# Kernel optimization log

Measured on AMD Instinct MI355X. Metric: run time of the kernel, lower is better.

The kernel has to match this reference:

```python
import jax, jax.numpy as jnp
import numpy as np

C = 512
REDUCTION = 8
POOLED_LEN = 256


def setup_inputs() -> dict:
    key = jax.random.key(0)
    k_x, k_w1, k_b1, k_w2, k_b2 = jax.random.split(key, 5)
    B, H, W = 32, 64, 64
    hid = C // REDUCTION  # 64
    fan1 = C + POOLED_LEN  # 768
    x = jax.random.normal(k_x, (B, C, H, W), dtype=jnp.float32)
    # torch nn.Linear default init: U(-1/sqrt(fan_in), 1/sqrt(fan_in))
    lim1 = 1.0 / np.sqrt(fan1)
    lim2 = 1.0 / np.sqrt(hid)
    fc1_w = jax.random.uniform(k_w1, (hid, fan1), jnp.float32, -lim1, lim1)
    fc1_b = jax.random.uniform(k_b1, (hid,), jnp.float32, -lim1, lim1)
    fc2_w = jax.random.uniform(k_w2, (1, hid), jnp.float32, -lim2, lim2)
    fc2_b = jax.random.uniform(k_b2, (1,), jnp.float32, -lim2, lim2)
    return {"x": x, "fc1_w": fc1_w, "fc1_b": fc1_b, "fc2_w": fc2_w, "fc2_b": fc2_b}


def reference(x, fc1_w, fc1_b, fc2_w, fc2_b):
    B, Ch, H, W = x.shape
    # spatial mean pool -> channel descriptor [B, C]
    x_c = x.mean(axis=(2, 3))
    # outer-product channel affinity [B, C, C]
    affinity = x_c[:, :, None] * x_c[:, None, :]
    # concat affinity with its transpose along last dim -> [B, C, 2C]
    r_i = jnp.concatenate([affinity, jnp.swapaxes(affinity, 1, 2)], axis=2)
    # adaptive_avg_pool1d(2C -> pooled_len): 2C divisible by pooled_len,
    # so it's exact uniform window averaging
    win = (2 * Ch) // POOLED_LEN
    r_i_pooled = r_i.reshape(B, Ch, POOLED_LEN, win).mean(axis=-1)
    # x_c broadcast along dim 1 -> [B, C, C]
    x_pooled = jnp.broadcast_to(x_c[:, None, :], (B, Ch, Ch))
    att_input = jnp.concatenate([x_pooled, r_i_pooled], axis=2)  # [B, C, C+pooled_len]
    s = jax.nn.relu(jnp.einsum('bcf,hf->bch', att_input, fc1_w) + fc1_b)
    a = jax.nn.sigmoid(jnp.einsum('bch,oh->bco', s, fc2_w) + fc2_b)  # [B, C, 1]
    return x * a[:, :, :, None]  # [B, C, 1, 1] broadcast
```

## Files before the change

kernel.cpp:

```cpp
#include <hip/hip_runtime.h>
#include <math.h>


#define B_  32
#define C_  512
#define HW_ 4096
#define ROWS_ (B_ * C_)

__global__ __launch_bounds__(256) void k_rowmean(const float* __restrict__ x,
                                                 float* __restrict__ xc) {
    const int row = blockIdx.x;
    const float4* xr = (const float4*)(x + (size_t)row * HW_);
    const int tid = threadIdx.x;
    float s = 0.f;
#pragma unroll
    for (int k = 0; k < 4; ++k) {
        float4 v = xr[tid + k * 256];
        s += (v.x + v.y) + (v.z + v.w);
    }
#pragma unroll
    for (int off = 32; off > 0; off >>= 1) s += __shfl_down(s, off, 64);
    __shared__ float wsum[4];
    const int lane = tid & 63, wave = tid >> 6;
    if (lane == 0) wsum[wave] = s;
    __syncthreads();
    if (tid == 0) {
        float t = (wsum[0] + wsum[1]) + (wsum[2] + wsum[3]);
        xc[row] = t * (1.0f / (float)HW_);
    }
}

__global__ __launch_bounds__(256) void k_att(const float* __restrict__ xc,
                                             const float* __restrict__ fc1w,
                                             const float* __restrict__ fc1b,
                                             const float* __restrict__ fc2w,
                                             const float* __restrict__ fc2b,
                                             float* __restrict__ a) {
    const int b = blockIdx.x;
    const int tid = threadIdx.x;
    __shared__ float xcs[C_];
    __shared__ float qs[128];
    __shared__ float p1[256], p2[256];
    __shared__ float s1[64], s2[64], w2s[64];

    xcs[tid]       = xc[b * C_ + tid];
    xcs[tid + 256] = xc[b * C_ + 256 + tid];
    if (tid < 64) w2s[tid] = fc2w[tid];
    __syncthreads();

    if (tid < 128) {
        qs[tid] = (xcs[4 * tid] + xcs[4 * tid + 1] + xcs[4 * tid + 2] + xcs[4 * tid + 3]) * 0.25f;
    }
    __syncthreads();

    const int h = tid & 63, part = tid >> 6;
    const float* w = fc1w + h * 768;
    float t1 = 0.f, t2 = 0.f;
    {
        const int f0 = part * 128;
#pragma unroll 8
        for (int f = 0; f < 128; ++f) t1 += xcs[f0 + f] * w[f0 + f];
        const int m0 = part * 32;
#pragma unroll 8
        for (int m = 0; m < 32; ++m) t2 += qs[m0 + m] * (w[512 + m0 + m] + w[640 + m0 + m]);
    }
    p1[tid] = t1;
    p2[tid] = t2;
    __syncthreads();
    if (tid < 64) {
        s1[tid] = (p1[tid] + p1[tid + 64]) + (p1[tid + 128] + p1[tid + 192]) + fc1b[tid];
        s2[tid] = (p2[tid] + p2[tid + 64]) + (p2[tid + 128] + p2[tid + 192]);
    }
    __syncthreads();

    const float bias2 = fc2b[0];
    for (int c = tid; c < C_; c += 256) {
        const float xv = xcs[c];
        float acc = bias2;
#pragma unroll 8
        for (int hh = 0; hh < 64; ++hh) {
            float z = s1[hh] + xv * s2[hh];
            acc += w2s[hh] * (z > 0.f ? z : 0.f);
        }
        a[b * C_ + c] = 1.0f / (1.0f + __expf(-acc));
    }
}

__global__ __launch_bounds__(256) void k_scale(const float* __restrict__ x,
                                               const float* __restrict__ a,
                                               float* __restrict__ out) {
    const int row = blockIdx.x;
    const float s = a[row];
    const float4* xr = (const float4*)(x + (size_t)row * HW_);
    float4* outr = (float4*)(out + (size_t)row * HW_);
    const int tid = threadIdx.x;
#pragma unroll
    for (int k = 0; k < 4; ++k) {
        float4 v = xr[tid + k * 256];
        v.x *= s; v.y *= s; v.z *= s; v.w *= s;
        outr[tid + k * 256] = v;
    }
}

extern "C" void kernel_launch(void* const* d_in, const int* in_sizes, int n_in,
                              void* d_out, int out_size, void* d_ws, size_t ws_size,
                              hipStream_t stream) {
    const float* x     = (const float*)d_in[0];
    const float* fc1_w = (const float*)d_in[1];
    const float* fc1_b = (const float*)d_in[2];
    const float* fc2_w = (const float*)d_in[3];
    const float* fc2_b = (const float*)d_in[4];
    float* out = (float*)d_out;

    float* xc = (float*)d_ws;
    float* a  = xc + ROWS_;

    k_rowmean<<<ROWS_, 256, 0, stream>>>(x, xc);
    k_att<<<B_, 256, 0, stream>>>(xc, fc1_w, fc1_b, fc2_w, fc2_b, a);
    k_scale<<<ROWS_, 256, 0, stream>>>(x, a, out);
}
```

Before: 491.9 us.

## Fuse attention MLP into scale kernel and use wave-per-row reductions

```diff
diff --git a/kernel.cpp b/kernel.cpp
--- a/kernel.cpp
+++ b/kernel.cpp
@@ -7,41 +7,43 @@
 #define HW_ 4096
 #define ROWS_ (B_ * C_)
 
+typedef float f32x4 __attribute__((ext_vector_type(4)));
+
 __global__ __launch_bounds__(256) void k_rowmean(const float* __restrict__ x,
                                                  float* __restrict__ xc) {
-    const int row = blockIdx.x;
-    const float4* xr = (const float4*)(x + (size_t)row * HW_);
-    const int tid = threadIdx.x;
+    const int lane = threadIdx.x & 63;
+    const int wave = threadIdx.x >> 6;
+    const int row  = blockIdx.x * 4 + wave;
+    const f32x4* xr = (const f32x4*)(x + (size_t)row * HW_);
     float s = 0.f;
 #pragma unroll
-    for (int k = 0; k < 4; ++k) {
-        float4 v = xr[tid + k * 256];
-        s += (v.x + v.y) + (v.z + v.w);
+    for (int j = 0; j < 16; ++j) {
+        f32x4 v = xr[lane + j * 64];
+        s += (v[0] + v[1]) + (v[2] + v[3]);
     }
 #pragma unroll
     for (int off = 32; off > 0; off >>= 1) s += __shfl_down(s, off, 64);
-    __shared__ float wsum[4];
-    const int lane = tid & 63, wave = tid >> 6;
-    if (lane == 0) wsum[wave] = s;
-    __syncthreads();
-    if (tid == 0) {
-        float t = (wsum[0] + wsum[1]) + (wsum[2] + wsum[3]);
-        xc[row] = t * (1.0f / (float)HW_);
-    }
+    if (lane == 0) xc[row] = s * (1.0f / (float)HW_);
 }
 
-__global__ __launch_bounds__(256) void k_att(const float* __restrict__ xc,
-                                             const float* __restrict__ fc1w,
-                                             const float* __restrict__ fc1b,
-                                             const float* __restrict__ fc2w,
-                                             const float* __restrict__ fc2b,
-                                             float* __restrict__ a) {
-    const int b = blockIdx.x;
+__global__ __launch_bounds__(256) void k_att_scale(
+        const float* __restrict__ x,
+        const float* __restrict__ xc,
+        const float* __restrict__ fc1w,
+        const float* __restrict__ fc1b,
+        const float* __restrict__ fc2w,
+        const float* __restrict__ fc2b,
+        float* __restrict__ out) {
     const int tid = threadIdx.x;
+    const int row_lo = ROWS_ - (int)(blockIdx.x + 1) * 16;
+    const int b  = row_lo / C_;
+    const int c0 = row_lo % C_;
+
     __shared__ float xcs[C_];
     __shared__ float qs[128];
     __shared__ float p1[256], p2[256];
     __shared__ float s1[64], s2[64], w2s[64];
+    __shared__ float as[16];
 
     xcs[tid]       = xc[b * C_ + tid];
     xcs[tid + 256] = xc[b * C_ + 256 + tid];
@@ -49,23 +51,25 @@
     __syncthreads();
 
     if (tid < 128) {
-        qs[tid] = (xcs[4 * tid] + xcs[4 * tid + 1] + xcs[4 * tid + 2] + xcs[4 * tid + 3]) * 0.25f;
+        qs[tid] = (xcs[4 * tid] + xcs[4 * tid + 1] +
+                   xcs[4 * tid + 2] + xcs[4 * tid + 3]) * 0.25f;
     }
     __syncthreads();
 
-    const int h = tid & 63, part = tid >> 6;
-    const float* w = fc1w + h * 768;
-    float t1 = 0.f, t2 = 0.f;
     {
+        const int h = tid & 63, part = tid >> 6;
+        const float* w = fc1w + h * 768;
+        float t1 = 0.f, t2 = 0.f;
         const int f0 = part * 128;
 #pragma unroll 8
         for (int f = 0; f < 128; ++f) t1 += xcs[f0 + f] * w[f0 + f];
         const int m0 = part * 32;
 #pragma unroll 8
-        for (int m = 0; m < 32; ++m) t2 += qs[m0 + m] * (w[512 + m0 + m] + w[640 + m0 + m]);
+        for (int m = 0; m < 32; ++m)
+            t2 += qs[m0 + m] * (w[512 + m0 + m] + w[640 + m0 + m]);
+        p1[tid] = t1;
+        p2[tid] = t2;
     }
-    p1[tid] = t1;
-    p2[tid] = t2;
     __syncthreads();
     if (tid < 64) {
         s1[tid] = (p1[tid] + p1[tid + 64]) + (p1[tid + 128] + p1[tid + 192]) + fc1b[tid];
@@ -73,32 +77,32 @@
     }
     __syncthreads();
 
-    const float bias2 = fc2b[0];
-    for (int c = tid; c < C_; c += 256) {
-        const float xv = xcs[c];
-        float acc = bias2;
+    if (tid < 16) {
+        const float xv = xcs[c0 + tid];
+        float acc = fc2b[0];
 #pragma unroll 8
         for (int hh = 0; hh < 64; ++hh) {
             float z = s1[hh] + xv * s2[hh];
             acc += w2s[hh] * (z > 0.f ? z : 0.f);
         }
-        a[b * C_ + c] = 1.0f / (1.0f + __expf(-acc));
+        as[tid] = 1.0f / (1.0f + __expf(-acc));
     }
-}
+    __syncthreads();
 
-__global__ __launch_bounds__(256) void k_scale(const float* __restrict__ x,
-                                               const float* __restrict__ a,
-                                               float* __restrict__ out) {
-    const int row = blockIdx.x;
-    const float s = a[row];
-    const float4* xr = (const float4*)(x + (size_t)row * HW_);
-    float4* outr = (float4*)(out + (size_t)row * HW_);
-    const int tid = threadIdx.x;
+    const int lane = tid & 63, wave = tid >> 6;
 #pragma unroll
-    for (int k = 0; k < 4; ++k) {
-        float4 v = xr[tid + k * 256];
-        v.x *= s; v.y *= s; v.z *= s; v.w *= s;
-        outr[tid + k * 256] = v;
+    for (int r = 0; r < 4; ++r) {
+        const int ri  = wave * 4 + r;
+        const int row = row_lo + ri;
+        const float sc = as[ri];
+        const f32x4* xr  = (const f32x4*)(x + (size_t)row * HW_);
+        f32x4* outr      = (f32x4*)(out + (size_t)row * HW_);
+#pragma unroll
+        for (int j = 0; j < 16; ++j) {
+            f32x4 v = xr[lane + j * 64];
+            v *= sc;
+            __builtin_nontemporal_store(v, &outr[lane + j * 64]);
+        }
     }
 }
 
@@ -113,9 +117,7 @@
     float* out = (float*)d_out;
 
     float* xc = (float*)d_ws;
-    float* a  = xc + ROWS_;
 
-    k_rowmean<<<ROWS_, 256, 0, stream>>>(x, xc);
-    k_att<<<B_, 256, 0, stream>>>(xc, fc1_w, fc1_b, fc2_w, fc2_b, a);
-    k_scale<<<ROWS_, 256, 0, stream>>>(x, a, out);
+    k_rowmean<<<ROWS_ / 4, 256, 0, stream>>>(x, xc);
+    k_att_scale<<<ROWS_ / 16, 256, 0, stream>>>(x, xc, fc1_w, fc1_b, fc2_w, fc2_b, out);
 }
```

After: 498.7 us. Within noise of the previous version (+1.4%).
